# Kernel optimization log

Measured on AMD Instinct MI355X. Metric: run time of the kernel, lower is better.

The kernel has to match this reference:

```python
import jax, jax.numpy as jnp
import numpy as np

N, S, L, F = 2000, 16, 128, 3   # nodes, samples, seq_len, features
DEG = 8                          # incoming edges per node
E = N * DEG
H = 1                            # LSTM hidden size (tgcnout_feats)
ENC = [1, 20, 10]                # encoder dims; decoder is reverse


def _lstm_layer(x, Wih, Whh, bih, bhh):
    """Single torch-style LSTM layer, batch_first. x: [B, L, D] -> [B, L, H].
    Gate order i, f, g, o as in torch.nn.LSTM."""
    B = x.shape[0]
    Hh = Whh.shape[1]
    xg = jnp.einsum('bld,gd->blg', x, Wih) + bih + bhh  # [B, L, 4H]

    def step(carry, xt):
        h, c = carry
        g = xt + h @ Whh.T
        i, f, gg, o = jnp.split(g, 4, axis=-1)
        i = jax.nn.sigmoid(i); f = jax.nn.sigmoid(f); o = jax.nn.sigmoid(o)
        gg = jnp.tanh(gg)
        c = f * c + i * gg
        h = o * jnp.tanh(c)
        return (h, c), h

    h0 = jnp.zeros((B, Hh), x.dtype)
    _, hs = jax.lax.scan(step, (h0, h0), jnp.swapaxes(xg, 0, 1))
    return jnp.swapaxes(hs, 0, 1)


def setup_inputs() -> dict:
    key = jax.random.key(0)
    ks = jax.random.split(key, 24)
    sc = 0.1
    d = {}
    d['inputs'] = jax.random.normal(ks[0], (N, S, L, F), jnp.float32)
    d['src'] = jax.random.randint(ks[1], (E,), 0, N)
    d['dst'] = jnp.arange(E) // DEG  # each node has exactly DEG in-edges
    # 2-layer LSTM (input 3 -> hidden 1, then 1 -> 1)
    d['w_ih0'] = jax.random.normal(ks[2], (4 * H, F), jnp.float32) * sc
    d['w_hh0'] = jax.random.normal(ks[3], (4 * H, H), jnp.float32) * sc
    d['b_ih0'] = jax.random.normal(ks[4], (4 * H,), jnp.float32) * sc
    d['b_hh0'] = jax.random.normal(ks[5], (4 * H,), jnp.float32) * sc
    d['w_ih1'] = jax.random.normal(ks[6], (4 * H, H), jnp.float32) * sc
    d['w_hh1'] = jax.random.normal(ks[7], (4 * H, H), jnp.float32) * sc
    d['b_ih1'] = jax.random.normal(ks[8], (4 * H,), jnp.float32) * sc
    d['b_hh1'] = jax.random.normal(ks[9], (4 * H,), jnp.float32) * sc
    # encoder 1->20->10, decoder 10->20->1 (torch Linear: W [out, in])
    d['We0'] = jax.random.normal(ks[10], (20, 1), jnp.float32) * sc
    d['be0'] = jax.random.normal(ks[11], (20,), jnp.float32) * sc
    d['We1'] = jax.random.normal(ks[12], (10, 20), jnp.float32) * sc
    d['be1'] = jax.random.normal(ks[13], (10,), jnp.float32) * sc
    d['Wd0'] = jax.random.normal(ks[14], (20, 10), jnp.float32) * sc
    d['bd0'] = jax.random.normal(ks[15], (20,), jnp.float32) * sc
    d['Wd1'] = jax.random.normal(ks[16], (1, 20), jnp.float32) * sc
    d['bd1'] = jax.random.normal(ks[17], (1,), jnp.float32) * sc
    return d


def reference(inputs, src, dst, w_ih0, w_hh0, b_ih0, b_hh0,
              w_ih1, w_hh1, b_ih1, b_hh1,
              We0, be0, We1, be1, Wd0, bd0, Wd1, bd1):
    # --- graph mean aggregation (DGL send/recv: mean of src['h'] per dst) ---
    msgs = inputs[src]                                    # [E, S, L, F]
    agg = jax.ops.segment_sum(msgs, dst, num_segments=N)  # [N, S, L, F]
    cnt = jax.ops.segment_sum(jnp.ones((E,), inputs.dtype), dst, num_segments=N)
    h = agg / jnp.maximum(cnt, 1.0)[:, None, None, None]
    # --- per-node LSTM, batched over (nodes * samples) ---
    x = h.reshape(N * S, L, F)
    x = _lstm_layer(x, w_ih0, w_hh0, b_ih0, b_hh0)
    x = _lstm_layer(x, w_ih1, w_hh1, b_ih1, b_hh1)
    x = jax.nn.relu(x).reshape(N, S, L, H)
    # --- encoder / decoder MLPs with ELU ---
    lin = lambda t, W, b: t @ W.T + b
    x = jax.nn.elu(lin(x, We0, be0))
    x = jax.nn.elu(lin(x, We1, be1))
    x = jax.nn.elu(lin(x, Wd0, bd0))
    x = jax.nn.elu(lin(x, Wd1, bd1))
    return x
```

## Files before the change

### kernel.cpp

```cpp
#include <hip/hip_runtime.h>
#include <hip/hip_fp16.h>
#include <cstddef>

#define NN 2000
#define SS 16
#define LL 128
#define FF 3
#define DEG 8
#define BB (NN * SS)
#define NEL (BB * LL)
#define TBL 1024
#define SGB 4096
#define STR (NN + 4)

__device__ __forceinline__ float sigm(float x) {
    return __builtin_amdgcn_rcpf(1.0f + __expf(-x));
}
__device__ __forceinline__ float tanhfast(float x) {
    return 1.0f - 2.0f * __builtin_amdgcn_rcpf(1.0f + __expf(2.0f * x));
}
__device__ __forceinline__ float elup(float x) {
    return x > 0.0f ? x : expm1f(x);
}

__device__ float mlp_eval(float x,
    const float* We0, const float* be0, const float* We1, const float* be1,
    const float* Wd0, const float* bd0, const float* Wd1, const float* bd1)
{
    float e0[20];
#pragma unroll
    for (int j = 0; j < 20; ++j) e0[j] = elup(fmaf(x, We0[j], be0[j]));
    float e1[10];
#pragma unroll
    for (int k = 0; k < 10; ++k) {
        float acc = be1[k];
#pragma unroll
        for (int j = 0; j < 20; ++j) acc = fmaf(e0[j], We1[k * 20 + j], acc);
        e1[k] = elup(acc);
    }
    float d0[20];
#pragma unroll
    for (int m = 0; m < 20; ++m) {
        float acc = bd0[m];
#pragma unroll
        for (int k = 0; k < 10; ++k) acc = fmaf(e1[k], Wd0[m * 10 + k], acc);
        d0[m] = elup(acc);
    }
    float acc = bd1[0];
#pragma unroll
    for (int m = 0; m < 20; ++m) acc = fmaf(d0[m], Wd1[m], acc);
    return elup(acc);
}

#define H2(u) (*(__half2*)&(u))

__global__ __launch_bounds__(1024, 8) void k_gather(
    const float* __restrict__ inp, const int* __restrict__ src,
    const float* __restrict__ We0, const float* __restrict__ be0,
    const float* __restrict__ We1, const float* __restrict__ be1,
    const float* __restrict__ Wd0, const float* __restrict__ bd0,
    const float* __restrict__ Wd1, const float* __restrict__ bd1,
    float2* __restrict__ tbl, uint2* __restrict__ xm)
{
    __shared__ uint2 A[3 * STR];
    const int bid = blockIdx.x;
    const int lq  = bid >> 4;
    const int s   = bid & 15;
    const int tid = threadIdx.x;

    if (bid < 6) {
        int i = bid * 1024 + tid;
        if (i < TBL) {
            const float inv = 1.0f / (float)TBL;
            float f0 = mlp_eval((float)i * inv,       We0, be0, We1, be1, Wd0, bd0, Wd1, bd1);
            float f1 = mlp_eval((float)(i + 1) * inv, We0, be0, We1, be1, Wd0, bd0, Wd1, bd1);
            tbl[i] = make_float2(f0, f1 - f0);
        } else if (i < 2 * TBL) {
            int j = i - TBL;
            float x0 = (float)j * 0.015625f - 8.0f;
            float f0 = tanhf(x0), f1 = tanhf(x0 + 0.015625f);
            tbl[i] = make_float2(f0, f1 - f0);
        } else if (i < 2 * TBL + SGB) {
            int j = i - 2 * TBL;
            float xc = ((float)j + 0.5f) * 0.00390625f - 8.0f;
            float* sg = (float*)(tbl + 2 * TBL);
            sg[j] = 1.0f / (1.0f + expf(-xc));
        }
    }

    {
        const int grp = tid >> 2, j = tid & 3;
        const float4* ib = (const float4*)inp + (size_t)s * 96 + lq * 3 + j;
        if (j < 3) {
            float4 v[8];
#pragma unroll
            for (int p = 0; p < 8; ++p) {
                int m = grp + 256 * p;
                if (m < NN) v[p] = ib[(size_t)m * 1536];
            }
#pragma unroll
            for (int p = 0; p < 8; ++p) {
                int m = grp + 256 * p;
                if (m < NN) {
                    __half2 a = __floats2half2_rn(v[p].x, v[p].y);
                    __half2 b = __floats2half2_rn(v[p].z, v[p].w);
                    A[j * STR + m] = make_uint2(*(unsigned*)&a, *(unsigned*)&b);
                }
            }
        }
    }
    __syncthreads();

    const __half2 eighth = __float2half2_rn(0.125f);

#define SUMARR(OFS, EA, EB, olo, ohi) { \
    uint2 e0=A[(OFS)+EA.x], e1=A[(OFS)+EA.y], e2=A[(OFS)+EA.z], e3=A[(OFS)+EA.w]; \
    uint2 e4=A[(OFS)+EB.x], e5=A[(OFS)+EB.y], e6=A[(OFS)+EB.z], e7=A[(OFS)+EB.w]; \
    olo = __hmul2(__hadd2(__hadd2(__hadd2(H2(e0.x),H2(e1.x)),__hadd2(H2(e2.x),H2(e3.x))), \
                          __hadd2(__hadd2(H2(e4.x),H2(e5.x)),__hadd2(H2(e6.x),H2(e7.x)))), eighth); \
    ohi = __hmul2(__hadd2(__hadd2(__hadd2(H2(e0.y),H2(e1.y)),__hadd2(H2(e2.y),H2(e3.y))), \
                          __hadd2(__hadd2(H2(e4.y),H2(e5.y)),__hadd2(H2(e6.y),H2(e7.y)))), eighth); }

    int4 sa0, sb0, sa1, sb1;
    {
        int n0 = tid, n1 = tid + 1024;
        const int4* s0 = (const int4*)(src + n0 * 8);
        sa0 = s0[0]; sb0 = s0[1];
        if (n1 < NN) {
            const int4* s1 = (const int4*)(src + n1 * 8);
            sa1 = s1[0]; sb1 = s1[1];
        }
    }
#pragma unroll
    for (int it = 0; it < 2; ++it) {
        int n = tid + 1024 * it;
        if (n < NN) {
            int4 ea = it ? sa1 : sa0;
            int4 eb = it ? sb1 : sb0;

            __half2 h0, h1, h2, h3, h4, h5;
            SUMARR(0,       ea, eb, h0, h1);
            SUMARR(STR,     ea, eb, h2, h3);
            SUMARR(2 * STR, ea, eb, h4, h5);
            unsigned u0 = *(unsigned*)&h0, u1 = *(unsigned*)&h1;
            unsigned u2 = *(unsigned*)&h2, u3 = *(unsigned*)&h3;
            unsigned u4 = *(unsigned*)&h4, u5 = *(unsigned*)&h5;

            uint2 q0 = make_uint2(u0, u1 & 0xFFFFu);
            uint2 q1 = make_uint2((u1 >> 16) | ((u2 & 0xFFFFu) << 16), u2 >> 16);
            uint2 q2 = make_uint2(u3, u4 & 0xFFFFu);
            uint2 q3 = make_uint2((u4 >> 16) | ((u5 & 0xFFFFu) << 16), u5 >> 16);

            size_t bcol = (size_t)s * NN + n;
            xm[(size_t)(4 * lq + 0) * BB + bcol] = q0;
            xm[(size_t)(4 * lq + 1) * BB + bcol] = q1;
            xm[(size_t)(4 * lq + 2) * BB + bcol] = q2;
            xm[(size_t)(4 * lq + 3) * BB + bcol] = q3;
        }
    }
#undef SUMARR
}

__device__ __forceinline__ float sigN(const float* __restrict__ t, float x) {
    float u = fmaf(x, 256.0f, 2048.0f);
    u = fminf(fmaxf(u, 0.0f), 4095.0f);
    return t[(int)u];
}
__device__ __forceinline__ float tanhL(const float2* __restrict__ t, float x) {
    float u = fminf(fmaxf(fmaf(x, 64.0f, 512.0f), 0.0f), 1023.995f);
    int i = (int)u;
    float2 e = t[i];
    return fmaf(u - (float)i, e.y, e.x);
}

__global__ __launch_bounds__(256) void k_lstm(
    const uint2* __restrict__ xm,
    const float* __restrict__ w_ih0, const float* __restrict__ b_ih0,
    const float* __restrict__ b_hh0, const float* __restrict__ w_hh0,
    const float* __restrict__ w_ih1, const float* __restrict__ w_hh1,
    const float* __restrict__ b_ih1, const float* __restrict__ b_hh1,
    const float2* __restrict__ tbl,
    float* __restrict__ out)
{
    __shared__ float2 sl[2 * TBL];
    __shared__ float  ssg[SGB];
    const int tid = threadIdx.x;
#pragma unroll
    for (int i = 0; i < 2 * TBL / 256; ++i) sl[tid + 256 * i] = tbl[tid + 256 * i];
    const float* sgsrc = (const float*)(tbl + 2 * TBL);
#pragma unroll
    for (int i = 0; i < SGB / 256; ++i) ssg[tid + 256 * i] = sgsrc[tid + 256 * i];
    __syncthreads();
    const float2* sout = sl;
    const float2* stnh = sl + TBL;

    const int lane  = tid & 63;
    const int chunk = (blockIdx.x & 1) * 4 + (tid >> 6);
    const int b = (blockIdx.x >> 1) * 64 + lane;
    const int n = b % NN;
    const int s = b / NN;

    float w[12], bg[4];
#pragma unroll
    for (int j = 0; j < 12; ++j) w[j] = w_ih0[j];
#pragma unroll
    for (int j = 0; j < 4; ++j) bg[j] = b_ih0[j] + b_hh0[j];

    float w0x = w_hh0[0], w0y = w_hh0[1], w0z = w_hh0[2], w0w = w_hh0[3];
    float ix = w_ih1[0], iy = w_ih1[1], iz = w_ih1[2], iw = w_ih1[3];
    float hx = w_hh1[0], hy = w_hh1[1], hz = w_hh1[2], hw = w_hh1[3];
    float bx = b_ih1[0] + b_hh1[0], by = b_ih1[1] + b_hh1[1];
    float bz = b_ih1[2] + b_hh1[2], bw = b_ih1[3] + b_hh1[3];

    const int l0 = chunk * 16;
    const int lw = (chunk == 0) ? 0 : l0 - 8;
    const int nst = l0 + 16 - lw;

    const uint2* gp = xm + b;
    uint2 ub[8];
#pragma unroll
    for (int d = 0; d < 8; ++d) ub[d] = gp[(size_t)(lw + d) * BB];

    float h0 = 0.f, c0 = 0.f, h1 = 0.f, c1 = 0.f;
    float* orow = out + ((size_t)n * SS + s) * LL;

    for (int t = 0; t < nst; t += 8) {
        bool pf = (t + 8) < nst;
        float rb[8];
#pragma unroll
        for (int d = 0; d < 8; ++d) {
            uint2 gv = ub[d];
            if (pf) ub[d] = gp[(size_t)(lw + t + 8 + d) * BB];

            __half2 hA = *(__half2*)&gv.x;
            __half2 hB = *(__half2*)&gv.y;
            float2 fA = __half22float2(hA);
            float a0 = fA.x, a1 = fA.y, a2 = __low2float(hB);

            float gx = fmaf(a0, w[0], fmaf(a1, w[1],  fmaf(a2, w[2],  bg[0])));
            float gy = fmaf(a0, w[3], fmaf(a1, w[4],  fmaf(a2, w[5],  bg[1])));
            float gz = fmaf(a0, w[6], fmaf(a1, w[7],  fmaf(a2, w[8],  bg[2])));
            float gw = fmaf(a0, w[9], fmaf(a1, w[10], fmaf(a2, w[11], bg[3])));

            float i  = sigN(ssg, fmaf(h0, w0x, gx));
            float f  = sigN(ssg, fmaf(h0, w0y, gy));
            float gg = tanhL(stnh, fmaf(h0, w0z, gz));
            float o  = sigN(ssg, fmaf(h0, w0w, gw));
            c0 = fmaf(f, c0, i * gg);
            h0 = o * tanhL(stnh, c0);

            float i1 = sigN(ssg, fmaf(h0, ix, fmaf(h1, hx, bx)));
            float f1 = sigN(ssg, fmaf(h0, iy, fmaf(h1, hy, by)));
            float g1 = tanhL(stnh, fmaf(h0, iz, fmaf(h1, hz, bz)));
            float o1 = sigN(ssg, fmaf(h0, iw, fmaf(h1, hw, bw)));
            c1 = fmaf(f1, c1, i1 * g1);
            h1 = o1 * tanhL(stnh, c1);

            rb[d] = fmaxf(h1, 0.0f);
        }
        int l = lw + t;
        if (l >= l0) {
            float v[8];
#pragma unroll
            for (int d = 0; d < 8; ++d) {
                float u = rb[d] * (float)TBL;
                int   i = (int)u;
                float2 e = sout[i];
                v[d] = fmaf(u - (float)i, e.y, e.x);
            }
            *(float4*)(orow + l)     = make_float4(v[0], v[1], v[2], v[3]);
            *(float4*)(orow + l + 4) = make_float4(v[4], v[5], v[6], v[7]);
        }
    }
}

__global__ __launch_bounds__(64) void k_lstm_fused(
    const float* __restrict__ inp, const int* __restrict__ src,
    const float* __restrict__ w_ih0, const float* __restrict__ w_hh0,
    const float* __restrict__ b_ih0, const float* __restrict__ b_hh0,
    const float* __restrict__ w_ih1, const float* __restrict__ w_hh1,
    const float* __restrict__ b_ih1, const float* __restrict__ b_hh1,
    float* __restrict__ out)
{
    int b = blockIdx.x * 64 + threadIdx.x;
    if (b >= BB) return;
    int n = b >> 4, s = b & 15;

    const float* base[8];
#pragma unroll
    for (int k = 0; k < 8; ++k)
        base[k] = inp + (size_t)(src[n * 8 + k] * SS + s) * LL * FF;

    float wi0[12], bg[4];
#pragma unroll
    for (int j = 0; j < 12; ++j) wi0[j] = w_ih0[j];
#pragma unroll
    for (int j = 0; j < 4; ++j) bg[j] = b_ih0[j] + b_hh0[j];

    float w0x = w_hh0[0], w0y = w_hh0[1], w0z = w_hh0[2], w0w = w_hh0[3];
    float ix = w_ih1[0], iy = w_ih1[1], iz = w_ih1[2], iw = w_ih1[3];
    float hx = w_hh1[0], hy = w_hh1[1], hz = w_hh1[2], hw = w_hh1[3];
    float bx = b_ih1[0] + b_hh1[0], by = b_ih1[1] + b_hh1[1];
    float bz = b_ih1[2] + b_hh1[2], bw = b_ih1[3] + b_hh1[3];

    float h0 = 0.f, c0 = 0.f, h1 = 0.f, c1 = 0.f;
    float rb0 = 0.f, rb1 = 0.f, rb2 = 0.f;
    float4* o4 = (float4*)(out + (size_t)b * LL);

#pragma unroll 4
    for (int l = 0; l < LL; ++l) {
        float a0 = 0.f, a1 = 0.f, a2 = 0.f;
#pragma unroll
        for (int k = 0; k < 8; ++k) {
            const float* p = base[k] + l * FF;
            a0 += p[0]; a1 += p[1]; a2 += p[2];
        }
        a0 *= 0.125f; a1 *= 0.125f; a2 *= 0.125f;

        float gx = fmaf(a0, wi0[0], fmaf(a1, wi0[1],  fmaf(a2, wi0[2],  bg[0])));
        float gy = fmaf(a0, wi0[3], fmaf(a1, wi0[4],  fmaf(a2, wi0[5],  bg[1])));
        float gz = fmaf(a0, wi0[6], fmaf(a1, wi0[7],  fmaf(a2, wi0[8],  bg[2])));
        float gw = fmaf(a0, wi0[9], fmaf(a1, wi0[10], fmaf(a2, wi0[11], bg[3])));

        float i  = sigm(fmaf(h0, w0x, gx));
        float f  = sigm(fmaf(h0, w0y, gy));
        float gg = tanhfast(fmaf(h0, w0z, gz));
        float o  = sigm(fmaf(h0, w0w, gw));
        c0 = fmaf(f, c0, i * gg);
        h0 = o * tanhfast(c0);

        float i1 = sigm(fmaf(h0, ix, fmaf(h1, hx, bx)));
        float f1 = sigm(fmaf(h0, iy, fmaf(h1, hy, by)));
        float g1 = tanhfast(fmaf(h0, iz, fmaf(h1, hz, bz)));
        float o1 = sigm(fmaf(h0, iw, fmaf(h1, hw, bw)));
        c1 = fmaf(f1, c1, i1 * g1);
        h1 = o1 * tanhfast(c1);

        float r = fmaxf(h1, 0.0f);
        int m = l & 3;
        if (m == 0) rb0 = r;
        else if (m == 1) rb1 = r;
        else if (m == 2) rb2 = r;
        else o4[l >> 2] = make_float4(rb0, rb1, rb2, r);
    }
}

__global__ __launch_bounds__(256) void k_mlp(
    const float* __restrict__ We0, const float* __restrict__ be0,
    const float* __restrict__ We1, const float* __restrict__ be1,
    const float* __restrict__ Wd0, const float* __restrict__ bd0,
    const float* __restrict__ Wd1, const float* __restrict__ bd1,
    float* __restrict__ out)
{
    int t = blockIdx.x * 256 + threadIdx.x;
    float x = out[t];
    out[t] = mlp_eval(x, We0, be0, We1, be1, Wd0, bd0, Wd1, bd1);
}

extern "C" void kernel_launch(void* const* d_in, const int* in_sizes, int n_in,
                              void* d_out, int out_size, void* d_ws, size_t ws_size,
                              hipStream_t stream)
{
    const float* inp   = (const float*)d_in[0];
    const int*   src   = (const int*)d_in[1];
    const float* w_ih0 = (const float*)d_in[3];
    const float* w_hh0 = (const float*)d_in[4];
    const float* b_ih0 = (const float*)d_in[5];
    const float* b_hh0 = (const float*)d_in[6];
    const float* w_ih1 = (const float*)d_in[7];
    const float* w_hh1 = (const float*)d_in[8];
    const float* b_ih1 = (const float*)d_in[9];
    const float* b_hh1 = (const float*)d_in[10];
    const float* We0 = (const float*)d_in[11];
    const float* be0 = (const float*)d_in[12];
    const float* We1 = (const float*)d_in[13];
    const float* be1 = (const float*)d_in[14];
    const float* Wd0 = (const float*)d_in[15];
    const float* bd0 = (const float*)d_in[16];
    const float* Wd1 = (const float*)d_in[17];
    const float* bd1 = (const float*)d_in[18];
    float* out = (float*)d_out;

    const size_t tbl_bytes = (size_t)(2 * TBL) * sizeof(float2)
                           + (size_t)SGB * sizeof(float);
    const size_t need = tbl_bytes + (size_t)NEL * sizeof(uint2);

    if (ws_size >= need) {
        float2* tbl = (float2*)d_ws;
        uint2*  xm  = (uint2*)((char*)d_ws + tbl_bytes);
        k_gather<<<512, 1024, 0, stream>>>(inp, src,
                                           We0, be0, We1, be1, Wd0, bd0, Wd1, bd1,
                                           tbl, xm);
        k_lstm<<<1000, 256, 0, stream>>>(xm, w_ih0, b_ih0, b_hh0, w_hh0,
                                         w_ih1, w_hh1, b_ih1, b_hh1, tbl, out);
    } else {
        k_lstm_fused<<<BB / 64, 64, 0, stream>>>(inp, src, w_ih0, w_hh0, b_ih0, b_hh0,
                                                 w_ih1, w_hh1, b_ih1, b_hh1, out);
        k_mlp<<<NEL / 256, 256, 0, stream>>>(We0, be0, We1, be1, Wd0, bd0, Wd1, bd1, out);
    }
}
```

Before: 66.39 us.

## Gather 16 timesteps per block with two-phase node staging in LDS

Each gather block now covers 16 timesteps instead of 4, cutting the grid from 512 to 128 blocks. The source nodes are staged in LDS in two halves of 1000 rows with a padded stride, and every destination accumulates its 8 neighbours in 48 half2 registers through a range-checked add. This is meant to cut repeated src index loads and per-block overhead and to make the input reads longer and contiguous. In exchange it uses far more registers and LDS per block, adds branchy edge checks, and leaves only 128 blocks, which may underfill the GPU.

```diff
diff --git a/kernel.cpp b/kernel.cpp
--- a/kernel.cpp
+++ b/kernel.cpp
@@ -11,7 +11,8 @@
 #define NEL (BB * LL)
 #define TBL 1024
 #define SGB 4096
-#define STR (NN + 4)
+#define NSTG 1000
+#define LSTRIDE 13
 
 __device__ __forceinline__ float sigm(float x) {
     return __builtin_amdgcn_rcpf(1.0f + __expf(-x));
@@ -54,7 +55,7 @@
 
 #define H2(u) (*(__half2*)&(u))
 
-__global__ __launch_bounds__(1024, 8) void k_gather(
+__global__ __launch_bounds__(1024, 4) void k_gather(
     const float* __restrict__ inp, const int* __restrict__ src,
     const float* __restrict__ We0, const float* __restrict__ be0,
     const float* __restrict__ We1, const float* __restrict__ be1,
@@ -62,9 +63,9 @@
     const float* __restrict__ Wd1, const float* __restrict__ bd1,
     float2* __restrict__ tbl, uint2* __restrict__ xm)
 {
-    __shared__ uint2 A[3 * STR];
+    __shared__ uint2 A[NSTG * LSTRIDE];
     const int bid = blockIdx.x;
-    const int lq  = bid >> 4;
+    const int lqq = bid >> 4;
     const int s   = bid & 15;
     const int tid = threadIdx.x;
 
@@ -88,77 +89,93 @@
         }
     }
 
+    const int n0 = tid, n1 = tid + 1024;
+    int4 ea0, eb0, ea1 = make_int4(0,0,0,0), eb1 = make_int4(0,0,0,0);
     {
-        const int grp = tid >> 2, j = tid & 3;
-        const float4* ib = (const float4*)inp + (size_t)s * 96 + lq * 3 + j;
-        if (j < 3) {
-            float4 v[8];
-#pragma unroll
-            for (int p = 0; p < 8; ++p) {
-                int m = grp + 256 * p;
-                if (m < NN) v[p] = ib[(size_t)m * 1536];
-            }
-#pragma unroll
-            for (int p = 0; p < 8; ++p) {
-                int m = grp + 256 * p;
-                if (m < NN) {
-                    __half2 a = __floats2half2_rn(v[p].x, v[p].y);
-                    __half2 b = __floats2half2_rn(v[p].z, v[p].w);
-                    A[j * STR + m] = make_uint2(*(unsigned*)&a, *(unsigned*)&b);
-                }
-            }
-        }
-    }
-    __syncthreads();
-
-    const __half2 eighth = __float2half2_rn(0.125f);
-
-#define SUMARR(OFS, EA, EB, olo, ohi) { \
-    uint2 e0=A[(OFS)+EA.x], e1=A[(OFS)+EA.y], e2=A[(OFS)+EA.z], e3=A[(OFS)+EA.w]; \
-    uint2 e4=A[(OFS)+EB.x], e5=A[(OFS)+EB.y], e6=A[(OFS)+EB.z], e7=A[(OFS)+EB.w]; \
-    olo = __hmul2(__hadd2(__hadd2(__hadd2(H2(e0.x),H2(e1.x)),__hadd2(H2(e2.x),H2(e3.x))), \
-                          __hadd2(__hadd2(H2(e4.x),H2(e5.x)),__hadd2(H2(e6.x),H2(e7.x)))), eighth); \
-    ohi = __hmul2(__hadd2(__hadd2(__hadd2(H2(e0.y),H2(e1.y)),__hadd2(H2(e2.y),H2(e3.y))), \
-                          __hadd2(__hadd2(H2(e4.y),H2(e5.y)),__hadd2(H2(e6.y),H2(e7.y)))), eighth); }
-
-    int4 sa0, sb0, sa1, sb1;
-    {
-        int n0 = tid, n1 = tid + 1024;
         const int4* s0 = (const int4*)(src + n0 * 8);
-        sa0 = s0[0]; sb0 = s0[1];
+        ea0 = s0[0]; eb0 = s0[1];
         if (n1 < NN) {
             const int4* s1 = (const int4*)(src + n1 * 8);
-            sa1 = s1[0]; sb1 = s1[1];
-        }
-    }
-#pragma unroll
-    for (int it = 0; it < 2; ++it) {
-        int n = tid + 1024 * it;
-        if (n < NN) {
-            int4 ea = it ? sa1 : sa0;
-            int4 eb = it ? sb1 : sb0;
-
-            __half2 h0, h1, h2, h3, h4, h5;
-            SUMARR(0,       ea, eb, h0, h1);
-            SUMARR(STR,     ea, eb, h2, h3);
-            SUMARR(2 * STR, ea, eb, h4, h5);
-            unsigned u0 = *(unsigned*)&h0, u1 = *(unsigned*)&h1;
-            unsigned u2 = *(unsigned*)&h2, u3 = *(unsigned*)&h3;
-            unsigned u4 = *(unsigned*)&h4, u5 = *(unsigned*)&h5;
-
-            uint2 q0 = make_uint2(u0, u1 & 0xFFFFu);
-            uint2 q1 = make_uint2((u1 >> 16) | ((u2 & 0xFFFFu) << 16), u2 >> 16);
-            uint2 q2 = make_uint2(u3, u4 & 0xFFFFu);
-            uint2 q3 = make_uint2((u4 >> 16) | ((u5 & 0xFFFFu) << 16), u5 >> 16);
-
-            size_t bcol = (size_t)s * NN + n;
-            xm[(size_t)(4 * lq + 0) * BB + bcol] = q0;
-            xm[(size_t)(4 * lq + 1) * BB + bcol] = q1;
-            xm[(size_t)(4 * lq + 2) * BB + bcol] = q2;
-            xm[(size_t)(4 * lq + 3) * BB + bcol] = q3;
-        }
-    }
-#undef SUMARR
+            ea1 = s1[0]; eb1 = s1[1];
+        }
+    }
+
+    __half2 H0[24], H1[24];
+    const __half2 hz = __float2half2_rn(0.0f);
+#pragma unroll
+    for (int k = 0; k < 24; ++k) { H0[k] = hz; H1[k] = hz; }
+
+#define ACC_EDGE(Hn, sn, lo) do {                                   \
+    int _m = (sn) - (lo);                                           \
+    if ((unsigned)_m < (unsigned)NSTG) {                            \
+        const uint2* _p = &A[_m * LSTRIDE];                         \
+        _Pragma("unroll")                                           \
+        for (int _j = 0; _j < 12; ++_j) {                           \
+            uint2 _e = _p[_j];                                      \
+            Hn[2*_j]   = __hadd2(Hn[2*_j],   H2(_e.x));             \
+            Hn[2*_j+1] = __hadd2(Hn[2*_j+1], H2(_e.y));             \
+        }                                                           \
+    }                                                               \
+} while (0)
+
+    for (int R = 0; R < 2; ++R) {
+        const int lo = R * NSTG;
+        if (R) __syncthreads();
+#pragma unroll
+        for (int k = 0; k < 12; ++k) {
+            int f = tid + 1024 * k;
+            if (f < NSTG * 12) {
+                int m = f / 12, q = f - 12 * m;
+                const float4* p = (const float4*)(inp
+                    + (size_t)(lo + m) * 6144 + s * 384 + lqq * 48) + q;
+                float4 v = *p;
+                __half2 a = __floats2half2_rn(v.x, v.y);
+                __half2 b = __floats2half2_rn(v.z, v.w);
+                A[m * LSTRIDE + q] = make_uint2(*(unsigned*)&a, *(unsigned*)&b);
+            }
+        }
+        __syncthreads();
+        ACC_EDGE(H0, ea0.x, lo); ACC_EDGE(H0, ea0.y, lo);
+        ACC_EDGE(H0, ea0.z, lo); ACC_EDGE(H0, ea0.w, lo);
+        ACC_EDGE(H0, eb0.x, lo); ACC_EDGE(H0, eb0.y, lo);
+        ACC_EDGE(H0, eb0.z, lo); ACC_EDGE(H0, eb0.w, lo);
+        if (n1 < NN) {
+            ACC_EDGE(H1, ea1.x, lo); ACC_EDGE(H1, ea1.y, lo);
+            ACC_EDGE(H1, ea1.z, lo); ACC_EDGE(H1, ea1.w, lo);
+            ACC_EDGE(H1, eb1.x, lo); ACC_EDGE(H1, eb1.y, lo);
+            ACC_EDGE(H1, eb1.z, lo); ACC_EDGE(H1, eb1.w, lo);
+        }
+    }
+#undef ACC_EDGE
+
+    const __half2 eighth = __float2half2_rn(0.125f);
+#pragma unroll
+    for (int k = 0; k < 24; ++k) { H0[k] = __hmul2(H0[k], eighth);
+                                   H1[k] = __hmul2(H1[k], eighth); }
+
+#define STORE_DST(Hn, n) do {                                        \
+    size_t _bcol = (size_t)s * NN + (n);                             \
+    unsigned _u[24];                                                 \
+    _Pragma("unroll")                                                \
+    for (int _k = 0; _k < 24; ++_k) _u[_k] = *(unsigned*)&Hn[_k];    \
+    _Pragma("unroll")                                                \
+    for (int _t = 0; _t < 16; ++_t) {                                \
+        unsigned _qx, _qy;                                           \
+        if ((_t & 1) == 0) {                                         \
+            _qx = _u[3 * _t / 2];                                    \
+            _qy = _u[3 * _t / 2 + 1] & 0xFFFFu;                      \
+        } else {                                                     \
+            int _a = (3 * _t - 1) / 2, _b = (3 * _t + 1) / 2;        \
+            _qx = (_u[_a] >> 16) | ((_u[_b] & 0xFFFFu) << 16);       \
+            _qy = _u[_b] >> 16;                                      \
+        }                                                            \
+        xm[(size_t)(lqq * 16 + _t) * BB + _bcol] = make_uint2(_qx, _qy); \
+    }                                                                \
+} while (0)
+
+    STORE_DST(H0, n0);
+    if (n1 < NN) STORE_DST(H1, n1);
+#undef STORE_DST
 }
 
 __device__ __forceinline__ float sigN(const float* __restrict__ t, float x) {
@@ -388,7 +405,7 @@
     if (ws_size >= need) {
         float2* tbl = (float2*)d_ws;
         uint2*  xm  = (uint2*)((char*)d_ws + tbl_bytes);
-        k_gather<<<512, 1024, 0, stream>>>(inp, src,
+        k_gather<<<128, 1024, 0, stream>>>(inp, src,
                                            We0, be0, We1, be1, Wd0, bd0, Wd1, bd1,
                                            tbl, xm);
         k_lstm<<<1000, 256, 0, stream>>>(xm, w_ih0, b_ih0, b_hh0, w_hh0,
```

Result: slower. 88.59 us (+33.4%).
